# Performance work log

Hardware: AMD Instinct MI355X
Metric: run time of the kernel (lower is better)

The kernel has to match this reference:

```python
import jax, jax.numpy as jnp
import numpy as np

B, S, D, H = 2, 2048, 1280, 16
DEPTH = D // H  # 80


def setup_inputs() -> dict:
    key = jax.random.key(0)
    ks = jax.random.split(key, 6)
    scale = 1.0 / np.sqrt(D)
    x = jax.random.normal(ks[0], (B, S, D), dtype=jnp.float32)
    # causal mask: 1.0 where attention is disallowed (strict upper triangle)
    mask = jnp.triu(jnp.ones((S, S), dtype=jnp.float32), k=1)
    Wq = jax.random.normal(ks[1], (D, D), dtype=jnp.float32) * scale
    Wk = jax.random.normal(ks[2], (D, D), dtype=jnp.float32) * scale
    Wv = jax.random.normal(ks[3], (D, D), dtype=jnp.float32) * scale
    Wo = jax.random.normal(ks[4], (D, D), dtype=jnp.float32) * scale
    z = jnp.zeros((D,), dtype=jnp.float32)
    return {"x": x, "mask": mask, "Wq": Wq, "bq": z, "Wk": Wk, "bk": z,
            "Wv": Wv, "bv": z, "Wo": Wo, "bo": z}


def _split_heads(t):
    # [B, S, D] -> [B, H, S, depth]
    return t.reshape(B, -1, H, DEPTH).transpose(0, 2, 1, 3)


def reference(x, mask, Wq, bq, Wk, bk, Wv, bv, Wo, bo):
    q = _split_heads(x @ Wq + bq)
    k = _split_heads(x @ Wk + bk)
    v = _split_heads(x @ Wv + bv)
    # scaled dot-product attention with additive (masked * -10000) logits
    logits = jnp.einsum("bhqd,bhkd->bhqk", q, k) / jnp.sqrt(
        jnp.asarray(DEPTH, dtype=jnp.float32))
    logits = logits + mask * -10000.0  # mask broadcasts over [B, H]
    attn = jax.nn.softmax(logits, axis=-1)
    ctx = jnp.einsum("bhqk,bhkd->bhqd", attn, v)
    ctx = ctx.transpose(0, 2, 1, 3).reshape(B, -1, D)  # merge heads
    return ctx @ Wo + bo
```

## Files before the change

kernel.cpp:

```cpp
#include <hip/hip_runtime.h>

typedef unsigned short u16;
typedef __bf16 bf16;
typedef __bf16 bf16x8 __attribute__((ext_vector_type(8)));
typedef unsigned short u16x8 __attribute__((ext_vector_type(8)));
typedef float f32x4 __attribute__((ext_vector_type(4)));

constexpr int B_ = 2, S_ = 2048, D_ = 1280, H_ = 16, DEPTH_ = 80;
constexpr int M_ = B_ * S_;
constexpr int QR_ = 128;

__device__ inline u16 f2b(float f) { return __builtin_bit_cast(u16, (bf16)f); }

typedef __attribute__((address_space(1))) const void gvoid;
typedef __attribute__((address_space(3))) void lvoid;
__device__ inline void gl_lds16(const void* g, void* l) {
  __builtin_amdgcn_global_load_lds((gvoid*)g, (lvoid*)l, 16, 0, 0);
}

__global__ __launch_bounds__(256) void prep_k(const float* __restrict__ x,
                                              u16* __restrict__ xbf,
                                              u16* __restrict__ QK,
                                              const float* __restrict__ W0,
                                              const float* __restrict__ W1,
                                              const float* __restrict__ W2,
                                              const float* __restrict__ W3,
                                              u16* __restrict__ WT) {
  __shared__ u16 t[32][33];
  int bid = blockIdx.x, tid = threadIdx.x;
  if (bid < 2560) {
    int i0 = (bid * 256 + tid) * 8;
    u16x8 v;
#pragma unroll
    for (int j = 0; j < 8; ++j) v[j] = f2b(x[i0 + j]);
    *(u16x8*)(xbf + i0) = v;
  } else if (bid < 5632) {
    int c = (bid - 2560) * 256 + tid;
    int r = c / 6, k = c - r * 6;
    u16x8 z = {};
    *(u16x8*)(QK + (size_t)r * QR_ + 80 + k * 8) = z;
  } else {
    int tt = bid - 5632;
    int z = tt / 1600, w = tt - z * 1600;
    int x0 = (w % 40) * 32, y0 = (w / 40) * 32;
    const float* srcs[4] = {W0, W1, W2, W3};
    const float* W = srcs[z];
    u16* out = WT + (size_t)z * D_ * D_;
    int tx = tid & 31, ty = tid >> 5;
#pragma unroll
    for (int i = 0; i < 4; ++i)
      t[ty + 8 * i][tx] = f2b(W[(size_t)(y0 + ty + 8 * i) * D_ + x0 + tx]);
    __syncthreads();
#pragma unroll
    for (int i = 0; i < 4; ++i)
      out[(size_t)(x0 + ty + 8 * i) * D_ + y0 + tx] = t[tx][ty + 8 * i];
  }
}

struct GemmAcc {
  f32x4 acc[4][4];
};
__device__ inline void gemm_core(const u16* __restrict__ A,
                                 const u16* __restrict__ BT, int m0, int n0,
                                 u16* a_s, u16* b_s, GemmAcc& g) {
  int tid = threadIdx.x, lane = tid & 63, wave = tid >> 6;
  int quad = lane >> 4, l15 = lane & 15;
  int wm = wave >> 1, wn = wave & 1;
  int r4 = lane >> 2, c4 = (lane & 3) * 8;

  for (int k0 = 0; k0 < D_; k0 += 32) {
    __syncthreads();
#pragma unroll
    for (int j = 0; j < 2; ++j) {
      int ch = wave * 2 + j;
      gl_lds16(A + (size_t)(m0 + ch * 16 + r4) * D_ + k0 + c4, a_s + ch * 512);
      gl_lds16(BT + (size_t)(n0 + ch * 16 + r4) * D_ + k0 + c4, b_s + ch * 512);
    }
    __syncthreads();
    bf16x8 af[4], bfr[4];
#pragma unroll
    for (int mt = 0; mt < 4; ++mt)
      af[mt] = *(const bf16x8*)(a_s + (wm * 64 + mt * 16 + l15) * 32 + quad * 8);
#pragma unroll
    for (int nt = 0; nt < 4; ++nt)
      bfr[nt] = *(const bf16x8*)(b_s + (wn * 64 + nt * 16 + l15) * 32 + quad * 8);
#pragma unroll
    for (int mt = 0; mt < 4; ++mt)
#pragma unroll
      for (int nt = 0; nt < 4; ++nt)
        g.acc[mt][nt] = __builtin_amdgcn_mfma_f32_16x16x32_bf16(
            af[mt], bfr[nt], g.acc[mt][nt], 0, 0, 0);
  }
}

__global__ __launch_bounds__(256, 4) void gemm_qkv(const u16* __restrict__ A,
                                                   const u16* __restrict__ BT,
                                                   const float* __restrict__ bq,
                                                   const float* __restrict__ bk,
                                                   const float* __restrict__ bv,
                                                   u16* __restrict__ Qw,
                                                   u16* __restrict__ Kw,
                                                   u16* __restrict__ Vw) {
  __shared__ __align__(16) u16 a_s[128 * 32];
  __shared__ __align__(16) u16 b_s[128 * 32];
  int lane = threadIdx.x & 63, wave = threadIdx.x >> 6;
  int quad = lane >> 4, l15 = lane & 15;
  int wm = wave >> 1, wn = wave & 1;
  int m0 = blockIdx.y * 128, n0 = blockIdx.x * 128;

  GemmAcc g = {};
  gemm_core(A, BT, m0, n0, a_s, b_s, g);

  int mat = n0 / D_;
  const float* bp = (mat == 0) ? bq : (mat == 1 ? bk : bv);
#pragma unroll
  for (int nt = 0; nt < 4; ++nt) {
    int ng = n0 + wn * 64 + nt * 16 + l15;
    int co = ng - mat * D_;
    float bv_ = bp[co];
    int h = co / DEPTH_, d = co % DEPTH_;
#pragma unroll
    for (int mt = 0; mt < 4; ++mt)
#pragma unroll
      for (int r = 0; r < 4; ++r) {
        int row = m0 + wm * 64 + mt * 16 + quad * 4 + r;
        int b = row >> 11, s = row & (S_ - 1);
        u16 bits = f2b(g.acc[mt][nt][r] + bv_);
        if (mat < 2) {
          u16* outp = mat ? Kw : Qw;
          outp[((size_t)(b * H_ + h) * S_ + s) * QR_ + d] = bits;
        } else {
          Vw[((size_t)(b * H_ + h) * DEPTH_ + d) * S_ + s] = bits;
        }
      }
  }
}

__global__ __launch_bounds__(256, 4) void gemm_out(const u16* __restrict__ A,
                                                   const u16* __restrict__ BT,
                                                   const float* __restrict__ bias,
                                                   float* __restrict__ out) {
  __shared__ __align__(16) u16 a_s[128 * 32];
  __shared__ __align__(16) u16 b_s[128 * 32];
  int lane = threadIdx.x & 63, wave = threadIdx.x >> 6;
  int quad = lane >> 4, l15 = lane & 15;
  int wm = wave >> 1, wn = wave & 1;
  int m0 = blockIdx.y * 128, n0 = blockIdx.x * 128;

  GemmAcc g = {};
  gemm_core(A, BT, m0, n0, a_s, b_s, g);

#pragma unroll
  for (int nt = 0; nt < 4; ++nt) {
    int col = n0 + wn * 64 + nt * 16 + l15;
    float bv = bias[col];
#pragma unroll
    for (int mt = 0; mt < 4; ++mt)
#pragma unroll
      for (int r = 0; r < 4; ++r) {
        int row = m0 + wm * 64 + mt * 16 + quad * 4 + r;
        out[(size_t)row * D_ + col] = g.acc[mt][nt][r] + bv;
      }
  }
}

__global__ __launch_bounds__(256, 4) void attn_k(const u16* __restrict__ Qp,
                                                 const u16* __restrict__ Kp,
                                                 const u16* __restrict__ VT,
                                                 u16* __restrict__ ctx) {
  constexpr float SCALE = 0.11180339887498949f;
  __shared__ __align__(16) u16 k_s[64 * 128];
  __shared__ __align__(16) u16 vt_s[80 * 64];
  __shared__ __align__(16) u16 p_s[64 * 72];
  int tid = threadIdx.x, lane = tid & 63, wave = tid >> 6;
  int quad = lane >> 4, l15 = lane & 15;
  int bx = blockIdx.x, by = blockIdx.y;
  int s_ = (by >> 4) & 1;
  int qt = s_ ? (31 - bx) : bx;
  int bh = (by & 15) | (((by >> 5) & 1) << 4);
  const u16* Qb = Qp + (size_t)bh * S_ * QR_;
  const u16* Kb = Kp + (size_t)bh * S_ * QR_;
  const u16* Vb = VT + (size_t)bh * DEPTH_ * S_;

  bf16x8 qf[3];
#pragma unroll
  for (int ks = 0; ks < 3; ++ks)
    qf[ks] = *(const bf16x8*)(Qb + (size_t)(qt * 64 + wave * 16 + l15) * QR_ +
                              ks * 32 + quad * 8);

  f32x4 acc_o[5] = {};
  float lsum[4] = {};

  for (int kt = 0; kt <= qt; ++kt) {
    int k0 = kt * 64;
    __syncthreads();
#pragma unroll
    for (int i = 0; i < 4; ++i) {
      int row = wave * 4 + quad + 16 * i;
      int sc = l15 ^ (row & 7);
      gl_lds16(Kb + (size_t)(k0 + row) * QR_ + sc * 8,
               k_s + (size_t)row * QR_ + l15 * 8);
    }
#pragma unroll
    for (int i = 0; i < 3; ++i) {
      int ch = tid + 256 * i;
      if (ch < 640) {
        int row = ch >> 3, pos = ch & 7;
        int sc = pos ^ (row & 7);
        gl_lds16(Vb + (size_t)row * S_ + k0 + sc * 8, vt_s + ch * 8);
      }
    }
    __syncthreads();

    f32x4 sa[4] = {};
#pragma unroll
    for (int ks = 0; ks < 3; ++ks) {
      int pa = ((ks * 4 + quad) ^ (l15 & 7)) * 8;
#pragma unroll
      for (int nt = 0; nt < 4; ++nt) {
        bf16x8 bfr = *(const bf16x8*)(k_s + (size_t)(nt * 16 + l15) * QR_ + pa);
        sa[nt] = __builtin_amdgcn_mfma_f32_16x16x32_bf16(qf[ks], bfr, sa[nt], 0, 0, 0);
      }
    }
    bool diag = (kt == qt);
#pragma unroll
    for (int nt = 0; nt < 4; ++nt)
#pragma unroll
      for (int r = 0; r < 4; ++r) {
        float p = __expf(sa[nt][r] * SCALE);
        if (diag && (nt * 16 + l15) > (wave * 16 + quad * 4 + r)) p = 0.0f;
        sa[nt][r] = p;
        lsum[r] += p;
      }
    asm volatile("s_waitcnt lgkmcnt(0)" ::: "memory");
#pragma unroll
    for (int nt = 0; nt < 4; ++nt)
#pragma unroll
      for (int r = 0; r < 4; ++r)
        p_s[(wave * 16 + quad * 4 + r) * 72 + nt * 16 + l15] = f2b(sa[nt][r]);
    asm volatile("s_waitcnt lgkmcnt(0)" ::: "memory");
#pragma unroll
    for (int kk = 0; kk < 2; ++kk) {
      bf16x8 af = *(const bf16x8*)(p_s + (wave * 16 + l15) * 72 + kk * 32 + quad * 8);
#pragma unroll
      for (int d5 = 0; d5 < 5; ++d5) {
        int pv = ((kk * 4 + quad) ^ (l15 & 7)) * 8;
        bf16x8 bfr = *(const bf16x8*)(vt_s + (size_t)(d5 * 16 + l15) * 64 + pv);
        acc_o[d5] = __builtin_amdgcn_mfma_f32_16x16x32_bf16(af, bfr, acc_o[d5], 0, 0, 0);
      }
    }
  }

#pragma unroll
  for (int r = 0; r < 4; ++r)
#pragma unroll
    for (int m = 1; m < 16; m <<= 1) lsum[r] += __shfl_xor(lsum[r], m, 16);

  int b = bh >> 4, h = bh & 15;
#pragma unroll
  for (int d5 = 0; d5 < 5; ++d5)
#pragma unroll
    for (int r = 0; r < 4; ++r) {
      int s = qt * 64 + wave * 16 + quad * 4 + r;
      int col = h * DEPTH_ + d5 * 16 + l15;
      ctx[(size_t)(b * S_ + s) * D_ + col] = f2b(acc_o[d5][r] / lsum[r]);
    }
}

extern "C" void kernel_launch(void* const* d_in, const int* in_sizes, int n_in,
                              void* d_out, int out_size, void* d_ws, size_t ws_size,
                              hipStream_t stream) {
  const float* x  = (const float*)d_in[0];
  const float* Wq = (const float*)d_in[2];
  const float* bq = (const float*)d_in[3];
  const float* Wk = (const float*)d_in[4];
  const float* bk = (const float*)d_in[5];
  const float* Wv = (const float*)d_in[6];
  const float* bv = (const float*)d_in[7];
  const float* Wo = (const float*)d_in[8];
  const float* bo = (const float*)d_in[9];

  const size_t DD = (size_t)D_ * D_;
  const size_t QE = (size_t)B_ * H_ * S_ * DEPTH_;
  const size_t QP = (size_t)B_ * H_ * S_ * QR_;
  u16* xbf = (u16*)d_ws;
  u16* wT  = xbf + QE;
  u16* Qw  = wT + 4 * DD;
  u16* Kw  = Qw + QP;
  u16* Vw  = Kw + QP;
  u16* Cw  = xbf;
  size_t need = (size_t)(Vw + QE - xbf) * 2;
  if (ws_size < need) return;

  prep_k<<<12032, 256, 0, stream>>>(x, xbf, Qw, Wq, Wk, Wv, Wo, wT);
  gemm_qkv<<<dim3(3 * D_ / 128, M_ / 128), 256, 0, stream>>>(xbf, wT, bq, bk, bv,
                                                             Qw, Kw, Vw);
  attn_k<<<dim3(16, 64), 256, 0, stream>>>(Qw, Kw, Vw, Cw);
  gemm_out<<<dim3(D_ / 128, M_ / 128), 256, 0, stream>>>(Cw, wT + 3 * DD, bo,
                                                         (float*)d_out);
}
```

Baseline: 273.5 us.

## Replace QKV GEMM with 256x256-tile, 8-wave, double-buffered pipelined kernel

Swaps the 128x128 QKV projection GEMM for a 256x256-tile kernel using 8 waves, 64-wide K steps and double-buffered LDS filled via direct global-to-LDS loads. The K loop is split into four MFMA phases, each interleaved with staging half of the next A or B tile, with barriers, setprio and explicit vmcnt waits to overlap memory with compute. LDS uses an XOR swizzle to avoid bank conflicts. The larger tiles raise data reuse but cut the grid to 15x16 blocks, which may underfill the GPU's compute units. The kernel also uses 128 KB of LDS per block.

```diff
diff --git a/kernel.cpp b/kernel.cpp
--- a/kernel.cpp
+++ b/kernel.cpp
@@ -93,49 +93,6 @@
   }
 }
 
-__global__ __launch_bounds__(256, 4) void gemm_qkv(const u16* __restrict__ A,
-                                                   const u16* __restrict__ BT,
-                                                   const float* __restrict__ bq,
-                                                   const float* __restrict__ bk,
-                                                   const float* __restrict__ bv,
-                                                   u16* __restrict__ Qw,
-                                                   u16* __restrict__ Kw,
-                                                   u16* __restrict__ Vw) {
-  __shared__ __align__(16) u16 a_s[128 * 32];
-  __shared__ __align__(16) u16 b_s[128 * 32];
-  int lane = threadIdx.x & 63, wave = threadIdx.x >> 6;
-  int quad = lane >> 4, l15 = lane & 15;
-  int wm = wave >> 1, wn = wave & 1;
-  int m0 = blockIdx.y * 128, n0 = blockIdx.x * 128;
-
-  GemmAcc g = {};
-  gemm_core(A, BT, m0, n0, a_s, b_s, g);
-
-  int mat = n0 / D_;
-  const float* bp = (mat == 0) ? bq : (mat == 1 ? bk : bv);
-#pragma unroll
-  for (int nt = 0; nt < 4; ++nt) {
-    int ng = n0 + wn * 64 + nt * 16 + l15;
-    int co = ng - mat * D_;
-    float bv_ = bp[co];
-    int h = co / DEPTH_, d = co % DEPTH_;
-#pragma unroll
-    for (int mt = 0; mt < 4; ++mt)
-#pragma unroll
-      for (int r = 0; r < 4; ++r) {
-        int row = m0 + wm * 64 + mt * 16 + quad * 4 + r;
-        int b = row >> 11, s = row & (S_ - 1);
-        u16 bits = f2b(g.acc[mt][nt][r] + bv_);
-        if (mat < 2) {
-          u16* outp = mat ? Kw : Qw;
-          outp[((size_t)(b * H_ + h) * S_ + s) * QR_ + d] = bits;
-        } else {
-          Vw[((size_t)(b * H_ + h) * DEPTH_ + d) * S_ + s] = bits;
-        }
-      }
-  }
-}
-
 __global__ __launch_bounds__(256, 4) void gemm_out(const u16* __restrict__ A,
                                                    const u16* __restrict__ BT,
                                                    const float* __restrict__ bias,
@@ -160,6 +117,171 @@
       for (int r = 0; r < 4; ++r) {
         int row = m0 + wm * 64 + mt * 16 + quad * 4 + r;
         out[(size_t)row * D_ + col] = g.acc[mt][nt][r] + bv;
+      }
+  }
+}
+
+__device__ inline void stage_half(const u16* __restrict__ gsrc, int half,
+                                  u16* lbase, int wave, int lane) {
+  int rl = lane >> 3, c8 = lane & 7;
+  int sc = (c8 ^ rl) << 3;
+#pragma unroll
+  for (int i = 0; i < 2; ++i) {
+    int j = half * 16 + wave * 2 + i;
+    gl_lds16(gsrc + (size_t)(j * 8 + rl) * D_ + sc, lbase + j * 512);
+  }
+}
+
+__device__ inline bf16x8 frd(const u16* b, int r, int g) {
+  return *(const bf16x8*)(b + r * 64 + ((g ^ (r & 7)) << 3));
+}
+
+__global__ __launch_bounds__(512, 2) void gemm_qkv8(
+    const u16* __restrict__ A, const u16* __restrict__ BT,
+    const float* __restrict__ bq, const float* __restrict__ bk,
+    const float* __restrict__ bv, u16* __restrict__ Qw, u16* __restrict__ Kw,
+    u16* __restrict__ Vw) {
+  __shared__ __align__(16) u16 AS[2][256 * 64];
+  __shared__ __align__(16) u16 BS[2][256 * 64];
+  constexpr int BK = 64, NT = D_ / BK;
+  int tid = threadIdx.x, lane = tid & 63, wave = tid >> 6;
+  int quad = lane >> 4, l15 = lane & 15;
+  int wm = wave >> 2, wn = wave & 3;
+  int m0 = blockIdx.y * 256, n0 = blockIdx.x * 256;
+  const u16* Ab = A + (size_t)m0 * D_;
+  const u16* Bb = BT + (size_t)n0 * D_;
+
+  f32x4 acc[8][4] = {};
+
+  stage_half(Ab, 0, (u16*)AS[0], wave, lane);
+  stage_half(Ab, 1, (u16*)AS[0], wave, lane);
+  stage_half(Bb, 0, (u16*)BS[0], wave, lane);
+  stage_half(Bb, 1, (u16*)BS[0], wave, lane);
+  stage_half(Bb + BK, 0, (u16*)BS[1], wave, lane);
+  stage_half(Bb + BK, 1, (u16*)BS[1], wave, lane);
+  asm volatile("s_waitcnt vmcnt(4)" ::: "memory");
+  __builtin_amdgcn_s_barrier();
+
+  bf16x8 a[4][2], bl[2][2], bh[2][2];
+  int ra = wm * 128 + l15, rb = wn * 64 + l15;
+
+#pragma unroll 2
+  for (int T = 0; T < NT; ++T) {
+    const u16* Ac = AS[T & 1];
+    const u16* Bc = BS[T & 1];
+    u16* An = (u16*)AS[(T + 1) & 1];
+    u16* Bcur = (u16*)BS[T & 1];
+
+#pragma unroll
+    for (int mt = 0; mt < 4; ++mt)
+#pragma unroll
+      for (int kh = 0; kh < 2; ++kh)
+        a[mt][kh] = frd(Ac, ra + mt * 16, kh * 4 + quad);
+#pragma unroll
+    for (int nt = 0; nt < 2; ++nt)
+#pragma unroll
+      for (int kh = 0; kh < 2; ++kh)
+        bl[nt][kh] = frd(Bc, rb + nt * 16, kh * 4 + quad);
+    if (T + 1 < NT) stage_half(Ab + (size_t)(T + 1) * BK, 0, An, wave, lane);
+    asm volatile("" ::: "memory");
+    __builtin_amdgcn_s_barrier();
+    __builtin_amdgcn_s_setprio(1);
+#pragma unroll
+    for (int mt = 0; mt < 4; ++mt)
+#pragma unroll
+      for (int nt = 0; nt < 2; ++nt)
+#pragma unroll
+        for (int kh = 0; kh < 2; ++kh)
+          acc[mt][nt] = __builtin_amdgcn_mfma_f32_16x16x32_bf16(
+              a[mt][kh], bl[nt][kh], acc[mt][nt], 0, 0, 0);
+    __builtin_amdgcn_s_setprio(0);
+    asm volatile("" ::: "memory");
+    __builtin_amdgcn_s_barrier();
+
+#pragma unroll
+    for (int nt = 0; nt < 2; ++nt)
+#pragma unroll
+      for (int kh = 0; kh < 2; ++kh)
+        bh[nt][kh] = frd(Bc, rb + 32 + nt * 16, kh * 4 + quad);
+    if (T + 1 < NT) stage_half(Ab + (size_t)(T + 1) * BK, 1, An, wave, lane);
+    asm volatile("" ::: "memory");
+    __builtin_amdgcn_s_barrier();
+    __builtin_amdgcn_s_setprio(1);
+#pragma unroll
+    for (int mt = 0; mt < 4; ++mt)
+#pragma unroll
+      for (int nt = 0; nt < 2; ++nt)
+#pragma unroll
+        for (int kh = 0; kh < 2; ++kh)
+          acc[mt][nt + 2] = __builtin_amdgcn_mfma_f32_16x16x32_bf16(
+              a[mt][kh], bh[nt][kh], acc[mt][nt + 2], 0, 0, 0);
+    __builtin_amdgcn_s_setprio(0);
+    asm volatile("" ::: "memory");
+    __builtin_amdgcn_s_barrier();
+
+#pragma unroll
+    for (int mt = 0; mt < 4; ++mt)
+#pragma unroll
+      for (int kh = 0; kh < 2; ++kh)
+        a[mt][kh] = frd(Ac, ra + 64 + mt * 16, kh * 4 + quad);
+    if (T + 2 < NT) stage_half(Bb + (size_t)(T + 2) * BK, 0, Bcur, wave, lane);
+    asm volatile("" ::: "memory");
+    __builtin_amdgcn_s_barrier();
+    __builtin_amdgcn_s_setprio(1);
+#pragma unroll
+    for (int mt = 0; mt < 4; ++mt)
+#pragma unroll
+      for (int nt = 0; nt < 2; ++nt)
+#pragma unroll
+        for (int kh = 0; kh < 2; ++kh)
+          acc[mt + 4][nt + 2] = __builtin_amdgcn_mfma_f32_16x16x32_bf16(
+              a[mt][kh], bh[nt][kh], acc[mt + 4][nt + 2], 0, 0, 0);
+    __builtin_amdgcn_s_setprio(0);
+    asm volatile("" ::: "memory");
+    __builtin_amdgcn_s_barrier();
+
+    if (T + 2 < NT) stage_half(Bb + (size_t)(T + 2) * BK, 1, Bcur, wave, lane);
+    asm volatile("" ::: "memory");
+    __builtin_amdgcn_s_barrier();
+    __builtin_amdgcn_s_setprio(1);
+#pragma unroll
+    for (int mt = 0; mt < 4; ++mt)
+#pragma unroll
+      for (int nt = 0; nt < 2; ++nt)
+#pragma unroll
+        for (int kh = 0; kh < 2; ++kh)
+          acc[mt + 4][nt] = __builtin_amdgcn_mfma_f32_16x16x32_bf16(
+              a[mt][kh], bl[nt][kh], acc[mt + 4][nt], 0, 0, 0);
+    __builtin_amdgcn_s_setprio(0);
+    if (T < NT - 2)
+      asm volatile("s_waitcnt vmcnt(4)" ::: "memory");
+    else if (T == NT - 2)
+      asm volatile("s_waitcnt vmcnt(0)" ::: "memory");
+    asm volatile("" ::: "memory");
+    __builtin_amdgcn_s_barrier();
+  }
+
+  int mat = n0 / D_;
+  const float* bp = (mat == 0) ? bq : (mat == 1 ? bk : bv);
+#pragma unroll
+  for (int nt = 0; nt < 4; ++nt) {
+    int ng = n0 + wn * 64 + nt * 16 + l15;
+    int co = ng - mat * D_;
+    float bb = bp[co];
+    int h = co / DEPTH_, d = co % DEPTH_;
+#pragma unroll
+    for (int mt = 0; mt < 8; ++mt)
+#pragma unroll
+      for (int r = 0; r < 4; ++r) {
+        int row = m0 + wm * 128 + mt * 16 + quad * 4 + r;
+        int b = row >> 11, s = row & (S_ - 1);
+        u16 bits = f2b(acc[mt][nt][r] + bb);
+        if (mat < 2) {
+          u16* outp = mat ? Kw : Qw;
+          outp[((size_t)(b * H_ + h) * S_ + s) * QR_ + d] = bits;
+        } else {
+          Vw[((size_t)(b * H_ + h) * DEPTH_ + d) * S_ + s] = bits;
+        }
       }
   }
 }
@@ -293,8 +415,8 @@
   if (ws_size < need) return;
 
   prep_k<<<12032, 256, 0, stream>>>(x, xbf, Qw, Wq, Wk, Wv, Wo, wT);
-  gemm_qkv<<<dim3(3 * D_ / 128, M_ / 128), 256, 0, stream>>>(xbf, wT, bq, bk, bv,
-                                                             Qw, Kw, Vw);
+  gemm_qkv8<<<dim3(3 * D_ / 256, M_ / 256), 512, 0, stream>>>(xbf, wT, bq, bk, bv,
+                                                              Qw, Kw, Vw);
   attn_k<<<dim3(16, 64), 256, 0, stream>>>(Qw, Kw, Vw, Cw);
   gemm_out<<<dim3(D_ / 128, M_ / 128), 256, 0, stream>>>(Cw, wT + 3 * DD, bo,
                                                          (float*)d_out);
```

Result: no change. 272.0 us (-0.6%).

## Replace QKV GEMM with 256x128 tile, 8-wave, triple-buffered LDS pipeline

Applied to the files above, without the earlier changes.

The QKV projection GEMM is rewritten as a 512-thread kernel computing 256x128 output tiles. It uses a three-stage LDS ring filled by direct global-to-LDS loads, with an XOR swizzle to avoid bank conflicts. A swizzled 1D block index improves L2 locality, and s_setprio is raised around the MFMA bursts. The aim is to hide global load latency and raise operand reuse per block, at the cost of more LDS per block (72 KB) and lower occupancy.

```diff
diff --git a/kernel.cpp b/kernel.cpp
--- a/kernel.cpp
+++ b/kernel.cpp
@@ -93,49 +93,6 @@
   }
 }
 
-__global__ __launch_bounds__(256, 4) void gemm_qkv(const u16* __restrict__ A,
-                                                   const u16* __restrict__ BT,
-                                                   const float* __restrict__ bq,
-                                                   const float* __restrict__ bk,
-                                                   const float* __restrict__ bv,
-                                                   u16* __restrict__ Qw,
-                                                   u16* __restrict__ Kw,
-                                                   u16* __restrict__ Vw) {
-  __shared__ __align__(16) u16 a_s[128 * 32];
-  __shared__ __align__(16) u16 b_s[128 * 32];
-  int lane = threadIdx.x & 63, wave = threadIdx.x >> 6;
-  int quad = lane >> 4, l15 = lane & 15;
-  int wm = wave >> 1, wn = wave & 1;
-  int m0 = blockIdx.y * 128, n0 = blockIdx.x * 128;
-
-  GemmAcc g = {};
-  gemm_core(A, BT, m0, n0, a_s, b_s, g);
-
-  int mat = n0 / D_;
-  const float* bp = (mat == 0) ? bq : (mat == 1 ? bk : bv);
-#pragma unroll
-  for (int nt = 0; nt < 4; ++nt) {
-    int ng = n0 + wn * 64 + nt * 16 + l15;
-    int co = ng - mat * D_;
-    float bv_ = bp[co];
-    int h = co / DEPTH_, d = co % DEPTH_;
-#pragma unroll
-    for (int mt = 0; mt < 4; ++mt)
-#pragma unroll
-      for (int r = 0; r < 4; ++r) {
-        int row = m0 + wm * 64 + mt * 16 + quad * 4 + r;
-        int b = row >> 11, s = row & (S_ - 1);
-        u16 bits = f2b(g.acc[mt][nt][r] + bv_);
-        if (mat < 2) {
-          u16* outp = mat ? Kw : Qw;
-          outp[((size_t)(b * H_ + h) * S_ + s) * QR_ + d] = bits;
-        } else {
-          Vw[((size_t)(b * H_ + h) * DEPTH_ + d) * S_ + s] = bits;
-        }
-      }
-  }
-}
-
 __global__ __launch_bounds__(256, 4) void gemm_out(const u16* __restrict__ A,
                                                    const u16* __restrict__ BT,
                                                    const float* __restrict__ bias,
@@ -160,6 +117,110 @@
       for (int r = 0; r < 4; ++r) {
         int row = m0 + wm * 64 + mt * 16 + quad * 4 + r;
         out[(size_t)row * D_ + col] = g.acc[mt][nt][r] + bv;
+      }
+  }
+}
+
+__device__ inline void stage32(const u16* __restrict__ gAk,
+                               const u16* __restrict__ gBk, u16* lbuf,
+                               int wave, int lane) {
+  int rl = lane >> 2;
+  int sg = ((lane & 3) ^ ((lane >> 3) & 3)) << 3;
+#pragma unroll
+  for (int i = 0; i < 3; ++i) {
+    int c = wave * 3 + i;
+    const u16* s = (c < 16) ? gAk + (size_t)(c * 16 + rl) * D_ + sg
+                            : gBk + (size_t)((c - 16) * 16 + rl) * D_ + sg;
+    gl_lds16(s, lbuf + c * 512);
+  }
+}
+
+__device__ inline bf16x8 frd32(const u16* buf, int r, int g) {
+  return *(const bf16x8*)(buf + r * 32 + ((g ^ ((r >> 1) & 3)) << 3));
+}
+
+__global__ __launch_bounds__(512, 4) void gemm_qkv8(
+    const u16* __restrict__ A, const u16* __restrict__ BT,
+    const float* __restrict__ bq, const float* __restrict__ bk,
+    const float* __restrict__ bv, u16* __restrict__ Qw, u16* __restrict__ Kw,
+    u16* __restrict__ Vw) {
+  __shared__ __align__(16) u16 LS[3 * 12288];
+  constexpr int NT = D_ / 32;
+  int tid = threadIdx.x, lane = tid & 63, wave = tid >> 6;
+  int quad = lane >> 4, l15 = lane & 15;
+  int wm = wave >> 1, wn = wave & 1;
+  int bid = blockIdx.x;
+  int sw = (bid & 7) * 60 + (bid >> 3);
+  int by = sw / 30, bx = sw - by * 30;
+  int m0 = by * 256, n0 = bx * 128;
+  const u16* Ab = A + (size_t)m0 * D_;
+  const u16* Bb = BT + (size_t)n0 * D_;
+
+  f32x4 acc[4][4] = {};
+
+  stage32(Ab, Bb, (u16*)LS, wave, lane);
+  stage32(Ab + 32, Bb + 32, (u16*)(LS + 12288), wave, lane);
+  asm volatile("s_waitcnt vmcnt(3)" ::: "memory");
+  __builtin_amdgcn_s_barrier();
+
+  int ra = wm * 64 + l15;
+  int rb = wn * 64 + l15;
+  int rdbuf = 0;
+  for (int T = 0; T < NT; ++T) {
+    const u16* cb = LS + rdbuf * 12288;
+    const u16* bbf = cb + 8192;
+    bf16x8 a[4], b[4];
+#pragma unroll
+    for (int mt = 0; mt < 4; ++mt) a[mt] = frd32(cb, ra + mt * 16, quad);
+#pragma unroll
+    for (int nt = 0; nt < 4; ++nt) b[nt] = frd32(bbf, rb + nt * 16, quad);
+    if (T + 2 < NT) {
+      int wb = rdbuf + 2;
+      if (wb >= 3) wb -= 3;
+      stage32(Ab + (size_t)(T + 2) * 32, Bb + (size_t)(T + 2) * 32,
+              (u16*)(LS + wb * 12288), wave, lane);
+    }
+    asm volatile("" ::: "memory");
+    __builtin_amdgcn_s_barrier();
+    __builtin_amdgcn_s_setprio(1);
+#pragma unroll
+    for (int mt = 0; mt < 4; ++mt)
+#pragma unroll
+      for (int nt = 0; nt < 4; ++nt)
+        acc[mt][nt] = __builtin_amdgcn_mfma_f32_16x16x32_bf16(
+            a[mt], b[nt], acc[mt][nt], 0, 0, 0);
+    __builtin_amdgcn_s_setprio(0);
+    if (T < NT - 2)
+      asm volatile("s_waitcnt vmcnt(3)" ::: "memory");
+    else
+      asm volatile("s_waitcnt vmcnt(0)" ::: "memory");
+    asm volatile("" ::: "memory");
+    __builtin_amdgcn_s_barrier();
+    rdbuf += 1;
+    if (rdbuf >= 3) rdbuf -= 3;
+  }
+
+  int mat = n0 / D_;
+  const float* bp = (mat == 0) ? bq : (mat == 1 ? bk : bv);
+#pragma unroll
+  for (int nt = 0; nt < 4; ++nt) {
+    int ng = n0 + wn * 64 + nt * 16 + l15;
+    int co = ng - mat * D_;
+    float bb_ = bp[co];
+    int h = co / DEPTH_, d = co % DEPTH_;
+#pragma unroll
+    for (int mt = 0; mt < 4; ++mt)
+#pragma unroll
+      for (int r = 0; r < 4; ++r) {
+        int row = m0 + wm * 64 + mt * 16 + quad * 4 + r;
+        int b = row >> 11, s = row & (S_ - 1);
+        u16 bits = f2b(acc[mt][nt][r] + bb_);
+        if (mat < 2) {
+          u16* outp = mat ? Kw : Qw;
+          outp[((size_t)(b * H_ + h) * S_ + s) * QR_ + d] = bits;
+        } else {
+          Vw[((size_t)(b * H_ + h) * DEPTH_ + d) * S_ + s] = bits;
+        }
       }
   }
 }
@@ -293,8 +354,7 @@
   if (ws_size < need) return;
 
   prep_k<<<12032, 256, 0, stream>>>(x, xbf, Qw, Wq, Wk, Wv, Wo, wT);
-  gemm_qkv<<<dim3(3 * D_ / 128, M_ / 128), 256, 0, stream>>>(xbf, wT, bq, bk, bv,
-                                                             Qw, Kw, Vw);
+  gemm_qkv8<<<480, 512, 0, stream>>>(xbf, wT, bq, bk, bv, Qw, Kw, Vw);
   attn_k<<<dim3(16, 64), 256, 0, stream>>>(Qw, Kw, Vw, Cw);
   gemm_out<<<dim3(D_ / 128, M_ / 128), 256, 0, stream>>>(Cw, wT + 3 * DD, bo,
                                                          (float*)d_out);
```

Result: slower. 280.8 us (+2.7%).
